# Performance work log

Hardware: AMD Instinct MI355X
Metric: run time of the kernel (lower is better)

The kernel has to match this reference:

```python
import jax, jax.numpy as jnp
import numpy as np

N_U = 100000   # num 'u' nodes
N_V = 100000   # num 'v' nodes (destination type)
D = 128        # feature dim
E1 = 3200000   # edges ('u','r1','v')
E2 = 3200000   # edges ('v','r2','v')


def setup_inputs() -> dict:
    key = jax.random.key(0)
    ks = jax.random.split(key, 10)
    inv = 1.0 / np.sqrt(D)
    inv3 = 1.0 / np.sqrt(3 * D)
    return {
        "x_u": jax.random.normal(ks[0], (N_U, D), jnp.float32),
        "x_v": jax.random.normal(ks[1], (N_V, D), jnp.float32),
        "W_r1": jax.random.normal(ks[2], (D, D), jnp.float32) * inv,
        "W_r2": jax.random.normal(ks[3], (D, D), jnp.float32) * inv,
        "W_gate": jax.random.normal(ks[4], (3 * D, 3 * D), jnp.float32) * inv3,
        "b_gate": jnp.zeros((3 * D,), jnp.float32),
        "W_aggr": jax.random.normal(ks[5], (3 * D, D), jnp.float32) * inv3,
        "b_aggr": jnp.zeros((D,), jnp.float32),
        "edge_index_r1": jax.random.randint(ks[6], (2, E1), 0, N_V, dtype=jnp.int64),
        "edge_index_r2": jax.random.randint(ks[7], (2, E2), 0, N_V, dtype=jnp.int64),
    }


def reference(x_u, x_v, W_r1, W_r2, W_gate, b_gate, W_aggr, b_aggr,
              edge_index_r1, edge_index_r2):
    n_v = x_v.shape[0]
    # per-edge-type conv: gather source features, per-relation linear message
    msg1 = x_u[edge_index_r1[0]] @ W_r1   # [E1, D]
    msg2 = x_v[edge_index_r2[0]] @ W_r2   # [E2, D]
    # concat all relations targeting dst 'v' (as in out_dict concatenation)
    msg = jnp.concatenate([msg1, msg2], axis=0)              # [E1+E2, D]
    idx = jnp.concatenate([edge_index_r1[1], edge_index_r2[1]])  # [E1+E2]
    # sum aggregation (scatter_add into zeros of shape [N_v, D])
    s = jax.ops.segment_sum(msg, idx, num_segments=n_v)
    # mean = sum / count.clamp(min=1)
    cnt = jax.ops.segment_sum(jnp.ones_like(msg), idx, num_segments=n_v)
    mean = s / jnp.clip(cnt, 1.0)
    # max with include_self=True over zero-initialized output -> max(msgs, 0), empty rows = 0
    mx = jnp.maximum(jax.ops.segment_max(msg, idx, num_segments=n_v), 0.0)
    total = jnp.concatenate([s, mean, mx], axis=1)           # [N_v, 3D]
    mask = jnp.sum(jnp.abs(total), axis=1) == 0              # untouched nodes
    gate = jax.nn.sigmoid(total @ W_gate + b_gate)           # attention gate
    out = (total * gate) @ W_aggr + b_aggr                   # [N_v, D]
    return jnp.where(mask[:, None], 0.0, out)
```

## Files before the change

kernel.cpp:

```cpp
#include <hip/hip_runtime.h>
#include <math.h>

#define N_U 100000
#define N_V 100000
#define D 128
#define E1 3200000
#define E2 3200000
#define ETOT (E1 + E2)

#define NBUCK 196
#define SLACK 35000
#define PCHUNK 4096
#define CSTRIDE 32

#define NBL_V 1563
#define NBL_U 1563
#define NBL_P 1563

typedef __bf16 bf16x8 __attribute__((ext_vector_type(8)));
typedef float f32x4 __attribute__((ext_vector_type(4)));

__device__ __forceinline__ unsigned short f2b(float f) {
  union { float f; unsigned int u; } v; v.f = f;
  unsigned int u = v.u;
  unsigned int r = u + 0x7fffu + ((u >> 16) & 1u);
  return (unsigned short)(r >> 16);
}
__device__ __forceinline__ float b2f(unsigned short s) {
  union { unsigned int u; float f; } v; v.u = ((unsigned int)s) << 16; return v.f;
}
__device__ __forceinline__ float b2f_lo(unsigned w) {
  union { unsigned u; float f; } v; v.u = w << 16; return v.f;
}
__device__ __forceinline__ float b2f_hi(unsigned w) {
  union { unsigned u; float f; } v; v.u = w & 0xffff0000u; return v.f;
}

__global__ __launch_bounds__(256) void convert_all(
    const float* __restrict__ W_r1, const float* __restrict__ W_r2,
    const float* __restrict__ W_gate, const float* __restrict__ W_aggr,
    unsigned short* __restrict__ Wr1F, unsigned short* __restrict__ Wr2F,
    unsigned short* __restrict__ WgF, unsigned short* __restrict__ WaF) {
  const int b = blockIdx.x;
  if (b < 128) {
    const float* W = (b < 64) ? W_r1 : W_r2;
    unsigned short* WF = (b < 64) ? Wr1F : Wr2F;
    int idx = (b & 63) * 256 + threadIdx.x;
    int k = idx >> 7, n = idx & 127;
    int f = (n >> 4) * 4 + (k >> 5);
    int out = f * 512 + ((n & 15) + 16 * ((k >> 3) & 3)) * 8 + (k & 7);
    WF[out] = f2b(W[k * 128 + n]);
  } else if (b < 704) {
    int idx = (b - 128) * 256 + threadIdx.x;
    int k = idx / 384, n = idx - k * 384;
    int f = (n >> 4) * 12 + (k >> 5);
    int out = f * 512 + ((n & 15) + 16 * ((k >> 3) & 3)) * 8 + (k & 7);
    WgF[out] = f2b(W_gate[k * 384 + n]);
  } else {
    int idx = (b - 704) * 256 + threadIdx.x;
    int k = idx >> 7, n = idx & 127;
    int f = (n >> 4) * 12 + (k >> 5);
    int out = f * 512 + ((n & 15) + 16 * ((k >> 3) & 3)) * 8 + (k & 7);
    WaF[out] = f2b(W_aggr[k * 128 + n]);
  }
}

#define LM 64
union SMem1 {
  struct { unsigned short Xs[LM][136]; } lin;
  struct {
    int hist[256]; int scan_s[256]; int lstart[256];
    int gbase[NBUCK]; int lcur[NBUCK];
    uint2 buf[PCHUNK];
  } part;
};

__device__ __forceinline__ void do_linear(
    const float* __restrict__ X, const unsigned short* __restrict__ WF,
    unsigned short* __restrict__ Hb, int nrows, int bid, SMem1& sm) {
  const int t = threadIdx.x;
  const int row0 = bid * LM;

  for (int i = t * 4; i < LM * 128; i += 1024) {
    int n = i >> 7, j = i & 127;
    int r = row0 + n;
    float4 v = make_float4(0.f, 0.f, 0.f, 0.f);
    if (r < nrows) v = *(const float4*)&X[(size_t)r * 128 + j];
    unsigned long long w =
        (unsigned long long)f2b(v.x) |
        ((unsigned long long)f2b(v.y) << 16) |
        ((unsigned long long)f2b(v.z) << 32) |
        ((unsigned long long)f2b(v.w) << 48);
    *(unsigned long long*)&sm.lin.Xs[n][j] = w;
  }
  __syncthreads();

  const int wv = t >> 6;
  const int ln = t & 63;
  const int lr = ln & 15;
  const int lq = ln >> 4;
  const int m0 = wv * 16;

  bf16x8 a[4];
#pragma unroll
  for (int ks = 0; ks < 4; ks++)
    a[ks] = *(const bf16x8*)&sm.lin.Xs[m0 + lr][ks * 32 + lq * 8];

#pragma unroll
  for (int np = 0; np < 4; np++) {
    const int n0 = np * 32;
    f32x4 acc0 = {0.f, 0.f, 0.f, 0.f};
    f32x4 acc1 = {0.f, 0.f, 0.f, 0.f};
    const unsigned short* B0 = WF + (size_t)(np * 2) * 4 * 512 + ln * 8;
    const unsigned short* B1 = B0 + 4 * 512;
#pragma unroll
    for (int ks = 0; ks < 4; ks++) {
      bf16x8 b0 = *(const bf16x8*)(B0 + ks * 512);
      bf16x8 b1 = *(const bf16x8*)(B1 + ks * 512);
      acc0 = __builtin_amdgcn_mfma_f32_16x16x32_bf16(a[ks], b0, acc0, 0, 0, 0);
      acc1 = __builtin_amdgcn_mfma_f32_16x16x32_bf16(a[ks], b1, acc1, 0, 0, 0);
    }
#pragma unroll
    for (int r = 0; r < 4; r++) {
      int grow = row0 + m0 + lq * 4 + r;
      if (grow < nrows) {
        Hb[(size_t)grow * 128 + n0 + lr] = f2b(acc0[r]);
        Hb[(size_t)grow * 128 + n0 + 16 + lr] = f2b(acc1[r]);
      }
    }
  }
}

__device__ __forceinline__ void do_partition(
    const int* __restrict__ e1, const int* __restrict__ e2,
    int* __restrict__ bucketCursor, uint2* __restrict__ recs,
    int bid, SMem1& sm) {
  const int t = threadIdx.x;
  const long base = (long)bid * PCHUNK;
  const int n = (int)min((long)PCHUNK, (long)ETOT - base);

  sm.part.hist[t] = 0;
  __syncthreads();

  uint2 myrec[PCHUNK / 256];
  int myb[PCHUNK / 256];
#pragma unroll
  for (int k = 0; k < PCHUNK / 256; k++) {
    int idx = t + k * 256;
    int enc = 0, dst = 0;
    if (idx < n) {
      long i = base + idx;
      if (i < E1) {
        dst = e1[E1 + i];
        enc = N_V + e1[i];
      } else {
        long j = i - E1;
        dst = e2[E2 + j];
        enc = e2[j];
      }
      atomicAdd(&sm.part.hist[dst >> 9], 1);
    }
    myrec[k] = make_uint2((unsigned)enc, (unsigned)dst);
    myb[k] = dst >> 9;
  }
  __syncthreads();

  int v = sm.part.hist[t];
  sm.part.scan_s[t] = v;
  __syncthreads();
  for (int off = 1; off < 256; off <<= 1) {
    int tmp = (t >= off) ? sm.part.scan_s[t - off] : 0;
    __syncthreads();
    sm.part.scan_s[t] += tmp;
    __syncthreads();
  }
  sm.part.lstart[t] = sm.part.scan_s[t] - v;
  if (t < NBUCK) {
    sm.part.gbase[t] = atomicAdd(&bucketCursor[t * CSTRIDE], v);
    sm.part.lcur[t] = sm.part.scan_s[t] - v;
  }
  __syncthreads();

#pragma unroll
  for (int k = 0; k < PCHUNK / 256; k++) {
    int idx = t + k * 256;
    if (idx < n) {
      int p = atomicAdd(&sm.part.lcur[myb[k]], 1);
      sm.part.buf[p] = myrec[k];
    }
  }
  __syncthreads();

  for (int p = t; p < n; p += 256) {
    uint2 r = sm.part.buf[p];
    int b = (int)(r.y >> 9);
    recs[(size_t)b * SLACK + sm.part.gbase[b] + (p - sm.part.lstart[b])] = r;
  }
}

__global__ __launch_bounds__(256) void stage1(
    const float* __restrict__ x_v, const float* __restrict__ x_u,
    const unsigned short* __restrict__ Wr2F, const unsigned short* __restrict__ Wr1F,
    unsigned short* __restrict__ Hb,
    const int* __restrict__ e1, const int* __restrict__ e2,
    int* __restrict__ bucketCursor, uint2* __restrict__ recs) {
  __shared__ SMem1 sm;
  const int b = blockIdx.x;
  if (b < NBL_V) {
    do_linear(x_v, Wr2F, Hb, N_V, b, sm);
  } else if (b < NBL_V + NBL_U) {
    do_linear(x_u, Wr1F, Hb + (size_t)N_V * D, N_U, b - NBL_V, sm);
  } else {
    do_partition(e1, e2, bucketCursor, recs, b - NBL_V - NBL_U, sm);
  }
}

__global__ __launch_bounds__(1024) void bucket_fill(
    const uint2* __restrict__ recs, const int* __restrict__ bucketCnt,
    int* __restrict__ row_ptr, int* __restrict__ col) {
  __shared__ int hist[512];
  __shared__ int s[512];
  __shared__ int curF[512];
  __shared__ int curB[512];
  __shared__ int sh_outBase;
  const int t = threadIdx.x;
  const int b = blockIdx.x;
  const size_t slack = (size_t)b * SLACK;
  const int n = bucketCnt[b * CSTRIDE];
  const int n0 = b << 9;

  int cv = 0;
  if (t < 256) {
    cv = (t < NBUCK) ? bucketCnt[t * CSTRIDE] : 0;
    s[t] = cv;
  }
  __syncthreads();
  for (int off = 1; off < 256; off <<= 1) {
    int tmp = 0;
    if (t < 256 && t >= off) tmp = s[t - off];
    __syncthreads();
    if (t < 256) s[t] += tmp;
    __syncthreads();
  }
  if (t == b) sh_outBase = s[t] - cv;
  __syncthreads();
  const int outBase = sh_outBase;

  if (t < 512) hist[t] = 0;
  __syncthreads();
  for (int p = t; p < n; p += 1024)
    atomicAdd(&hist[recs[slack + p].y - n0], 1);
  __syncthreads();

  int v = 0;
  if (t < 512) {
    v = hist[t];
    s[t] = v;
  }
  __syncthreads();
  for (int off = 1; off < 512; off <<= 1) {
    int tmp = 0;
    if (t < 512 && t >= off) tmp = s[t - off];
    __syncthreads();
    if (t < 512) s[t] += tmp;
    __syncthreads();
  }
  if (t < 512) {
    int excl = s[t] - v;
    curF[t] = excl;
    curB[t] = excl + v;
    int nd = n0 + t;
    if (nd < N_V) row_ptr[nd] = outBase + excl;
  }
  if (b == 0 && t == 0) row_ptr[N_V] = ETOT;
  __syncthreads();

  for (int p = t; p < n; p += 1024) {
    uint2 r = recs[slack + p];
    int local = r.y - n0;
    int q;
    if (r.x >= (unsigned)N_V) q = atomicSub(&curB[local], 1) - 1;
    else q = atomicAdd(&curF[local], 1);
    col[outBase + q] = (int)(r.x << 8);
  }
}

#define AGG1(w)                                        \
  do {                                                 \
    float lo = b2f_lo(w), hi = b2f_hi(w);              \
    s[2 * q] += lo; s[2 * q + 1] += hi;                \
    m[2 * q] = fmaxf(m[2 * q], lo);                    \
    m[2 * q + 1] = fmaxf(m[2 * q + 1], hi);            \
  } while (0)

__global__ __launch_bounds__(256) void aggregate_kernel(
    const unsigned short* __restrict__ Hb, const int* __restrict__ row_ptr,
    const int* __restrict__ col, unsigned int* __restrict__ SumB,
    unsigned int* __restrict__ MxB, int nodeBase) {
  const int node = nodeBase + blockIdx.x * 4 + (threadIdx.x >> 6);
  const int lane = threadIdx.x & 63;
  const int grp = lane >> 4;
  const int fl = lane & 15;
  const int start = row_ptr[node];
  const int end = row_ptr[node + 1];
  const char* Hc = (const char*)Hb;
  const int byteoff = fl * 16;

  float s[8] = {0.f, 0.f, 0.f, 0.f, 0.f, 0.f, 0.f, 0.f};
  float m[8] = {0.f, 0.f, 0.f, 0.f, 0.f, 0.f, 0.f, 0.f};

  int i = start;
  for (; i + 31 < end; i += 32) {
    uint4 v[8];
#pragma unroll
    for (int g = 0; g < 8; g++) {
      int e = i + g * 4 + grp;
      v[g] = *(const uint4*)(Hc + (unsigned)col[e] + byteoff);
    }
#pragma unroll
    for (int g = 0; g < 8; g++) {
      { int q = 0; AGG1(v[g].x); }
      { int q = 1; AGG1(v[g].y); }
      { int q = 2; AGG1(v[g].z); }
      { int q = 3; AGG1(v[g].w); }
    }
  }
  for (; i < end; i += 4) {
    int e = i + grp;
    int ec = e < end ? e : (end - 1);
    uint4 v = *(const uint4*)(Hc + (unsigned)col[ec] + byteoff);
    if (e >= end) { v.x = 0u; v.y = 0u; v.z = 0u; v.w = 0u; }
    { int q = 0; AGG1(v.x); }
    { int q = 1; AGG1(v.y); }
    { int q = 2; AGG1(v.z); }
    { int q = 3; AGG1(v.w); }
  }

#pragma unroll
  for (int k = 0; k < 8; k++) {
    s[k] += __shfl_xor(s[k], 16, 64);
    m[k] = fmaxf(m[k], __shfl_xor(m[k], 16, 64));
    s[k] += __shfl_xor(s[k], 32, 64);
    m[k] = fmaxf(m[k], __shfl_xor(m[k], 32, 64));
  }

  if (lane < 16) {
    uint4 o;
    o.x = (unsigned)f2b(s[0]) | ((unsigned)f2b(s[1]) << 16);
    o.y = (unsigned)f2b(s[2]) | ((unsigned)f2b(s[3]) << 16);
    o.z = (unsigned)f2b(s[4]) | ((unsigned)f2b(s[5]) << 16);
    o.w = (unsigned)f2b(s[6]) | ((unsigned)f2b(s[7]) << 16);
    ((uint4*)SumB)[(size_t)node * 16 + fl] = o;
  } else if (lane < 32) {
    uint4 o;
    o.x = (unsigned)f2b(m[0]) | ((unsigned)f2b(m[1]) << 16);
    o.y = (unsigned)f2b(m[2]) | ((unsigned)f2b(m[3]) << 16);
    o.z = (unsigned)f2b(m[4]) | ((unsigned)f2b(m[5]) << 16);
    o.w = (unsigned)f2b(m[6]) | ((unsigned)f2b(m[7]) << 16);
    ((uint4*)MxB)[(size_t)node * 16 + fl] = o;
  }
}

#define EM 64
__global__ __launch_bounds__(256, 3) void epilogue_mfma(
    const unsigned short* __restrict__ SumB, const unsigned short* __restrict__ MxB,
    const int* __restrict__ row_ptr, const unsigned short* __restrict__ WgF,
    const float* __restrict__ bg, const unsigned short* __restrict__ WaF,
    const float* __restrict__ ba, float* __restrict__ Out) {
  __shared__ unsigned short Ts[EM][392];
  __shared__ float invs[EM];
  __shared__ int cnts[EM];

  const int t = threadIdx.x;
  const int node0 = blockIdx.x * EM;

  if (t < EM) {
    int nd = node0 + t;
    int c = 0;
    if (nd < N_V) c = row_ptr[nd + 1] - row_ptr[nd];
    cnts[t] = c;
    invs[t] = 1.0f / (float)(c > 0 ? c : 1);
  }
  __syncthreads();

  {
    const uint4* Sv = (const uint4*)SumB;
    const uint4* Mv = (const uint4*)MxB;
    for (int i = t; i < EM * 16; i += 256) {
      int n = i >> 4, u = i & 15;
      int nd = node0 + n;
      uint4 s = make_uint4(0u, 0u, 0u, 0u);
      uint4 m4 = make_uint4(0u, 0u, 0u, 0u);
      if (nd < N_V) {
        s = Sv[(size_t)nd * 16 + u];
        m4 = Mv[(size_t)nd * 16 + u];
      }
      float inv = invs[n];
      *(uint4*)&Ts[n][u * 8] = s;
      unsigned sw[4] = {s.x, s.y, s.z, s.w};
      unsigned mr[4];
#pragma unroll
      for (int q = 0; q < 4; q++) {
        unsigned short lo = f2b(b2f((unsigned short)sw[q]) * inv);
        unsigned short hi = f2b(b2f((unsigned short)(sw[q] >> 16)) * inv);
        mr[q] = (unsigned)lo | ((unsigned)hi << 16);
      }
      *(uint4*)&Ts[n][128 + u * 8] = make_uint4(mr[0], mr[1], mr[2], mr[3]);
      *(uint4*)&Ts[n][256 + u * 8] = m4;
    }
  }
  __syncthreads();

  const int wv = t >> 6;
  const int ln = t & 63;
  const int lr = ln & 15;
  const int lq = ln >> 4;

  f32x4 acc[4][6];
#pragma unroll
  for (int m = 0; m < 4; m++)
#pragma unroll
    for (int nt = 0; nt < 6; nt++) acc[m][nt] = (f32x4){0.f, 0.f, 0.f, 0.f};

  const unsigned short* Bg = WgF + (size_t)(wv * 6) * 12 * 512 + ln * 8;

#pragma unroll 2
  for (int kc = 0; kc < 12; kc++) {
    bf16x8 b[6];
#pragma unroll
    for (int nt = 0; nt < 6; nt++)
      b[nt] = *(const bf16x8*)(Bg + (nt * 12 + kc) * 512);
    bf16x8 a[4];
#pragma unroll
    for (int m = 0; m < 4; m++)
      a[m] = *(const bf16x8*)&Ts[m * 16 + lr][kc * 32 + lq * 8];
#pragma unroll
    for (int m = 0; m < 4; m++)
#pragma unroll
      for (int nt = 0; nt < 6; nt++)
        acc[m][nt] = __builtin_amdgcn_mfma_f32_16x16x32_bf16(a[m], b[nt], acc[m][nt], 0, 0, 0);
  }
  __syncthreads();

#pragma unroll
  for (int nt = 0; nt < 6; nt++) {
    int cg = wv * 96 + nt * 16 + lr;
    float bgv = bg[cg];
#pragma unroll
    for (int m = 0; m < 4; m++) {
#pragma unroll
      for (int r = 0; r < 4; r++) {
        int row = m * 16 + lq * 4 + r;
        float g = 1.f / (1.f + __expf(-(acc[m][nt][r] + bgv)));
        Ts[row][cg] = f2b(b2f(Ts[row][cg]) * g);
      }
    }
  }
  __syncthreads();

  f32x4 acc2[4][2];
#pragma unroll
  for (int m = 0; m < 4; m++)
#pragma unroll
    for (int nt = 0; nt < 2; nt++) acc2[m][nt] = (f32x4){0.f, 0.f, 0.f, 0.f};

  const unsigned short* Ba = WaF + (size_t)(wv * 2) * 12 * 512 + ln * 8;

#pragma unroll 2
  for (int kc = 0; kc < 12; kc++) {
    bf16x8 b[2];
#pragma unroll
    for (int nt = 0; nt < 2; nt++)
      b[nt] = *(const bf16x8*)(Ba + (nt * 12 + kc) * 512);
    bf16x8 a[4];
#pragma unroll
    for (int m = 0; m < 4; m++)
      a[m] = *(const bf16x8*)&Ts[m * 16 + lr][kc * 32 + lq * 8];
#pragma unroll
    for (int m = 0; m < 4; m++)
#pragma unroll
      for (int nt = 0; nt < 2; nt++)
        acc2[m][nt] = __builtin_amdgcn_mfma_f32_16x16x32_bf16(a[m], b[nt], acc2[m][nt], 0, 0, 0);
  }

#pragma unroll
  for (int nt = 0; nt < 2; nt++) {
    int cg = wv * 32 + nt * 16 + lr;
    float bav = ba[cg];
#pragma unroll
    for (int m = 0; m < 4; m++) {
#pragma unroll
      for (int r = 0; r < 4; r++) {
        int row = m * 16 + lq * 4 + r;
        int nd = node0 + row;
        if (nd < N_V) {
          float msk = (cnts[row] > 0) ? 1.f : 0.f;
          Out[(size_t)nd * D + cg] = (acc2[m][nt][r] + bav) * msk;
        }
      }
    }
  }
}

extern "C" void kernel_launch(void* const* d_in, const int* in_sizes, int n_in,
                              void* d_out, int out_size, void* d_ws, size_t ws_size,
                              hipStream_t stream) {
  const float* x_u = (const float*)d_in[0];
  const float* x_v = (const float*)d_in[1];
  const float* W_r1 = (const float*)d_in[2];
  const float* W_r2 = (const float*)d_in[3];
  const float* W_gate = (const float*)d_in[4];
  const float* b_gate = (const float*)d_in[5];
  const float* W_aggr = (const float*)d_in[6];
  const float* b_aggr = (const float*)d_in[7];
  const int* e1 = (const int*)d_in[8];
  const int* e2 = (const int*)d_in[9];
  float* out = (float*)d_out;

  char* ws = (char*)d_ws;
  size_t off = 0;
  unsigned short* Hb = (unsigned short*)(ws + off); off += (size_t)(N_V + N_U) * D * 2;
  unsigned int* SumB = (unsigned int*)(ws + off);   off += (size_t)N_V * D * 2;
  unsigned int* MxB = (unsigned int*)(ws + off);    off += (size_t)N_V * D * 2;
  int* colA = (int*)(ws + off);        off += (size_t)ETOT * 4;
  uint2* recs = (uint2*)(ws + off);    off += (size_t)NBUCK * SLACK * 8;
  int* row_ptr = (int*)(ws + off);     off += (size_t)(N_V + 1) * 4;
  int* bucketCursor = (int*)(ws + off); off += (size_t)NBUCK * CSTRIDE * 4;
  unsigned short* Wg16 = (unsigned short*)(ws + off); off += (size_t)384 * 384 * 2;
  unsigned short* Wa16 = (unsigned short*)(ws + off); off += (size_t)128 * 384 * 2;
  unsigned short* Wr1T = (unsigned short*)(ws + off); off += (size_t)128 * 128 * 2;
  unsigned short* Wr2T = (unsigned short*)(ws + off); off += (size_t)128 * 128 * 2;

  hipMemsetAsync(bucketCursor, 0, (size_t)NBUCK * CSTRIDE * 4, stream);

  convert_all<<<896, 256, 0, stream>>>(W_r1, W_r2, W_gate, W_aggr,
                                       Wr1T, Wr2T, Wg16, Wa16);

  stage1<<<NBL_V + NBL_U + NBL_P, 256, 0, stream>>>(
      x_v, x_u, Wr2T, Wr1T, Hb, e1, e2, bucketCursor, recs);

  bucket_fill<<<NBUCK, 1024, 0, stream>>>(recs, bucketCursor, row_ptr, colA);

  aggregate_kernel<<<N_V / 8, 256, 0, stream>>>(Hb, row_ptr, colA, SumB, MxB, 0);
  aggregate_kernel<<<N_V / 8, 256, 0, stream>>>(Hb, row_ptr, colA, SumB, MxB, N_V / 2);

  epilogue_mfma<<<(N_V + EM - 1) / EM, 256, 0, stream>>>(
      (const unsigned short*)SumB, (const unsigned short*)MxB, row_ptr,
      Wg16, b_gate, Wa16, b_aggr, out);
}
```

Measured before the change: 604.5 us.

## Pack partition records to 32 bits, stage linear output through LDS, reorder blocks

Each edge record now packs the source encoding and the low 9 bits of the destination into one 32-bit word, with the bucket implied by its slot. This halves record traffic between the partition and bucket_fill stages. The linear-transform output is written to shared memory first and then copied to global memory with coalesced 16-byte stores, replacing scattered 2-byte stores. Partition blocks are also moved ahead of the linear blocks in stage1, so the atomic-heavy partition work starts earliest; the cost is an extra LDS round trip and two barriers per linear block.

```diff
diff --git a/kernel.cpp b/kernel.cpp
--- a/kernel.cpp
+++ b/kernel.cpp
@@ -105,6 +105,7 @@
 #pragma unroll
   for (int ks = 0; ks < 4; ks++)
     a[ks] = *(const bf16x8*)&sm.lin.Xs[m0 + lr][ks * 32 + lq * 8];
+  __syncthreads();
 
 #pragma unroll
   for (int np = 0; np < 4; np++) {
@@ -122,18 +123,31 @@
     }
 #pragma unroll
     for (int r = 0; r < 4; r++) {
-      int grow = row0 + m0 + lq * 4 + r;
-      if (grow < nrows) {
-        Hb[(size_t)grow * 128 + n0 + lr] = f2b(acc0[r]);
-        Hb[(size_t)grow * 128 + n0 + 16 + lr] = f2b(acc1[r]);
-      }
+      int row = m0 + lq * 4 + r;
+      sm.lin.Xs[row][n0 + lr] = f2b(acc0[r]);
+      sm.lin.Xs[row][n0 + 16 + lr] = f2b(acc1[r]);
+    }
+  }
+  __syncthreads();
+
+  {
+    int row = t >> 2, part = t & 3;
+    int grow = row0 + row;
+    if (grow < nrows) {
+      uint4* dst = (uint4*)&Hb[(size_t)grow * 128 + part * 32];
+      const unsigned short* src = &sm.lin.Xs[row][part * 32];
+      uint4 w0 = *(const uint4*)(src);
+      uint4 w1 = *(const uint4*)(src + 8);
+      uint4 w2 = *(const uint4*)(src + 16);
+      uint4 w3 = *(const uint4*)(src + 24);
+      dst[0] = w0; dst[1] = w1; dst[2] = w2; dst[3] = w3;
     }
   }
 }
 
 __device__ __forceinline__ void do_partition(
     const int* __restrict__ e1, const int* __restrict__ e2,
-    int* __restrict__ bucketCursor, uint2* __restrict__ recs,
+    int* __restrict__ bucketCursor, unsigned* __restrict__ recs,
     int bid, SMem1& sm) {
   const int t = threadIdx.x;
   const long base = (long)bid * PCHUNK;
@@ -160,7 +174,8 @@
       }
       atomicAdd(&sm.part.hist[dst >> 9], 1);
     }
-    myrec[k] = make_uint2((unsigned)enc, (unsigned)dst);
+    myrec[k] = make_uint2(((unsigned)enc << 9) | ((unsigned)dst & 511u),
+                          (unsigned)(dst >> 9));
     myb[k] = dst >> 9;
   }
   __syncthreads();
@@ -193,8 +208,8 @@
 
   for (int p = t; p < n; p += 256) {
     uint2 r = sm.part.buf[p];
-    int b = (int)(r.y >> 9);
-    recs[(size_t)b * SLACK + sm.part.gbase[b] + (p - sm.part.lstart[b])] = r;
+    int b = (int)r.y;
+    recs[(size_t)b * SLACK + sm.part.gbase[b] + (p - sm.part.lstart[b])] = r.x;
   }
 }
 
@@ -203,20 +218,20 @@
     const unsigned short* __restrict__ Wr2F, const unsigned short* __restrict__ Wr1F,
     unsigned short* __restrict__ Hb,
     const int* __restrict__ e1, const int* __restrict__ e2,
-    int* __restrict__ bucketCursor, uint2* __restrict__ recs) {
+    int* __restrict__ bucketCursor, unsigned* __restrict__ recs) {
   __shared__ SMem1 sm;
   const int b = blockIdx.x;
-  if (b < NBL_V) {
-    do_linear(x_v, Wr2F, Hb, N_V, b, sm);
-  } else if (b < NBL_V + NBL_U) {
-    do_linear(x_u, Wr1F, Hb + (size_t)N_V * D, N_U, b - NBL_V, sm);
+  if (b < NBL_P) {
+    do_partition(e1, e2, bucketCursor, recs, b, sm);
+  } else if (b < NBL_P + NBL_V) {
+    do_linear(x_v, Wr2F, Hb, N_V, b - NBL_P, sm);
   } else {
-    do_partition(e1, e2, bucketCursor, recs, b - NBL_V - NBL_U, sm);
+    do_linear(x_u, Wr1F, Hb + (size_t)N_V * D, N_U, b - NBL_P - NBL_V, sm);
   }
 }
 
 __global__ __launch_bounds__(1024) void bucket_fill(
-    const uint2* __restrict__ recs, const int* __restrict__ bucketCnt,
+    const unsigned* __restrict__ recs, const int* __restrict__ bucketCnt,
     int* __restrict__ row_ptr, int* __restrict__ col) {
   __shared__ int hist[512];
   __shared__ int s[512];
@@ -228,6 +243,7 @@
   const size_t slack = (size_t)b * SLACK;
   const int n = bucketCnt[b * CSTRIDE];
   const int n0 = b << 9;
+  (void)n0;
 
   int cv = 0;
   if (t < 256) {
@@ -249,7 +265,7 @@
   if (t < 512) hist[t] = 0;
   __syncthreads();
   for (int p = t; p < n; p += 1024)
-    atomicAdd(&hist[recs[slack + p].y - n0], 1);
+    atomicAdd(&hist[recs[slack + p] & 511u], 1);
   __syncthreads();
 
   int v = 0;
@@ -269,19 +285,20 @@
     int excl = s[t] - v;
     curF[t] = excl;
     curB[t] = excl + v;
-    int nd = n0 + t;
+    int nd = (b << 9) + t;
     if (nd < N_V) row_ptr[nd] = outBase + excl;
   }
   if (b == 0 && t == 0) row_ptr[N_V] = ETOT;
   __syncthreads();
 
   for (int p = t; p < n; p += 1024) {
-    uint2 r = recs[slack + p];
-    int local = r.y - n0;
+    unsigned r = recs[slack + p];
+    int local = (int)(r & 511u);
+    unsigned enc = r >> 9;
     int q;
-    if (r.x >= (unsigned)N_V) q = atomicSub(&curB[local], 1) - 1;
+    if (enc >= (unsigned)N_V) q = atomicSub(&curB[local], 1) - 1;
     else q = atomicAdd(&curF[local], 1);
-    col[outBase + q] = (int)(r.x << 8);
+    col[outBase + q] = (int)(enc << 8);
   }
 }
 
@@ -523,7 +540,7 @@
   unsigned int* SumB = (unsigned int*)(ws + off);   off += (size_t)N_V * D * 2;
   unsigned int* MxB = (unsigned int*)(ws + off);    off += (size_t)N_V * D * 2;
   int* colA = (int*)(ws + off);        off += (size_t)ETOT * 4;
-  uint2* recs = (uint2*)(ws + off);    off += (size_t)NBUCK * SLACK * 8;
+  unsigned* recs = (unsigned*)(ws + off); off += (size_t)NBUCK * SLACK * 4;
   int* row_ptr = (int*)(ws + off);     off += (size_t)(N_V + 1) * 4;
   int* bucketCursor = (int*)(ws + off); off += (size_t)NBUCK * CSTRIDE * 4;
   unsigned short* Wg16 = (unsigned short*)(ws + off); off += (size_t)384 * 384 * 2;
@@ -536,7 +553,7 @@
   convert_all<<<896, 256, 0, stream>>>(W_r1, W_r2, W_gate, W_aggr,
                                        Wr1T, Wr2T, Wg16, Wa16);
 
-  stage1<<<NBL_V + NBL_U + NBL_P, 256, 0, stream>>>(
+  stage1<<<NBL_P + NBL_V + NBL_U, 256, 0, stream>>>(
       x_v, x_u, Wr2T, Wr1T, Hb, e1, e2, bucketCursor, recs);
 
   bucket_fill<<<NBUCK, 1024, 0, stream>>>(recs, bucketCursor, row_ptr, colA);
```

Result: faster. 577.4 us (-4.5%).
